# Kernel optimization log

Measured on AMD Instinct MI355X. Metric: run time of the kernel, lower is better.

Reference implementation:

```python
import jax, jax.numpy as jnp
import numpy as np

C_Z = 128
C_H = 128
N = 512
B = 1

def _layer_norm(x, g, b, eps=1e-5):
    mu = jnp.mean(x, axis=-1, keepdims=True)
    var = jnp.var(x, axis=-1, keepdims=True)
    return (x - mu) * jax.lax.rsqrt(var + eps) * g + b

def _linear(x, w, b):
    # torch Linear: y = x @ w.T + b, w: [out, in]
    return jnp.einsum('...i,oi->...o', x, w) + b

def setup_inputs() -> dict:
    key = jax.random.key(0)
    ks = jax.random.split(key, 8)
    s = 1.0 / np.sqrt(C_Z)
    return {
        'z': jax.random.normal(ks[0], (B, N, N, C_Z), jnp.float32),
        'mask': jnp.ones((B, N, N), jnp.float32),
        'ln_in_g': jnp.ones((C_Z,), jnp.float32),
        'ln_in_b': jnp.zeros((C_Z,), jnp.float32),
        'w_ag': jax.random.normal(ks[1], (C_H, C_Z), jnp.float32) * s,
        'b_ag': jnp.ones((C_H,), jnp.float32),
        'w_ap': jax.random.normal(ks[2], (C_H, C_Z), jnp.float32) * s,
        'b_ap': jnp.zeros((C_H,), jnp.float32),
        'w_bg': jax.random.normal(ks[3], (C_H, C_Z), jnp.float32) * s,
        'b_bg': jnp.ones((C_H,), jnp.float32),
        'w_bp': jax.random.normal(ks[4], (C_H, C_Z), jnp.float32) * s,
        'b_bp': jnp.zeros((C_H,), jnp.float32),
        'w_g': jax.random.normal(ks[5], (C_Z, C_Z), jnp.float32) * s,
        'b_g': jnp.zeros((C_Z,), jnp.float32),
        'w_z': jax.random.normal(ks[6], (C_Z, C_H), jnp.float32) * s,
        'b_z': jnp.zeros((C_Z,), jnp.float32),
        'ln_out_g': jnp.ones((C_H,), jnp.float32),
        'ln_out_b': jnp.zeros((C_H,), jnp.float32),
    }

def reference(z, mask, ln_in_g, ln_in_b, w_ag, b_ag, w_ap, b_ap,
              w_bg, b_bg, w_bp, b_bp, w_g, b_g, w_z, b_z,
              ln_out_g, ln_out_b):
    m = mask[..., None]                       # [B,N,N,1]
    zn = _layer_norm(z, ln_in_g, ln_in_b)     # [B,N,N,Cz]
    a = m * jax.nn.sigmoid(_linear(zn, w_ag, b_ag)) * _linear(zn, w_ap, b_ap)
    b = m * jax.nn.sigmoid(_linear(zn, w_bg, b_bg)) * _linear(zn, w_bp, b_bp)
    # outgoing: x[b,i,j,c] = sum_k a[b,i,k,c] * b[b,j,k,c]
    x = jnp.einsum('bikc,bjkc->bijc', a, b)
    x = _layer_norm(x, ln_out_g, ln_out_b)
    x = _linear(x, w_z, b_z)
    g = jax.nn.sigmoid(_linear(zn, w_g, b_g))
    return x * g
```

## Files before the change

kernel.cpp:

```cpp
#include <hip/hip_runtime.h>

#define NN 512
#define CCH 128
#define MM (NN*NN)

using f32x4  = __attribute__((ext_vector_type(4))) float;
using f32x2  = __attribute__((ext_vector_type(2))) float;
using bf16x8 = __attribute__((ext_vector_type(8))) short;
using u16x4  = __attribute__((ext_vector_type(4))) unsigned short;
typedef unsigned short u16;

__device__ __forceinline__ u16 f2bf(float f) {
    unsigned u = __builtin_bit_cast(unsigned, f);
    u += 0x7FFF + ((u >> 16) & 1);
    return (u16)(u >> 16);
}
__device__ __forceinline__ float bf2f(u16 h) {
    unsigned u = ((unsigned)h) << 16;
    return __builtin_bit_cast(float, u);
}
__device__ __forceinline__ float sigm(float x) { return 1.0f / (1.0f + __expf(-x)); }

__device__ __forceinline__ void gl_lds16(const void* g, void* l) {
    __builtin_amdgcn_global_load_lds(
        (const __attribute__((address_space(1))) void*)g,
        (__attribute__((address_space(3))) void*)l, 16, 0, 0);
}

__global__ __launch_bounds__(256) void k_prep(
    const float* __restrict__ w0, const float* __restrict__ w1,
    const float* __restrict__ w2, const float* __restrict__ w3,
    const float* __restrict__ w4, const float* __restrict__ w5,
    const float* __restrict__ b0, const float* __restrict__ b1,
    const float* __restrict__ b2, const float* __restrict__ b3,
    const float* __restrict__ b4, const float* __restrict__ b5,
    const float* __restrict__ gin, const float* __restrict__ bin,
    const float* __restrict__ gout, const float* __restrict__ bout,
    u16* __restrict__ wbf, float* __restrict__ bias2) {
    int mat = blockIdx.x;
    const float* W = mat==0?w0:mat==1?w1:mat==2?w2:mat==3?w3:mat==4?w4:w5;
    const float* B = mat==0?b0:mat==1?b1:mat==2?b2:mat==3?b3:mat==4?b4:b5;
    const float* G = (mat==5)? gout : gin;
    const float* Bt= (mat==5)? bout : bin;
    __shared__ float gs[CCH], bs[CCH];
    int tid = threadIdx.x;
    if (tid < CCH) { gs[tid] = G[tid]; bs[tid] = Bt[tid]; }
    __syncthreads();
    int o = tid >> 1, c0 = (tid & 1) * 64;
    const float* src = W + o * CCH + c0;
    char* dstrow = (char*)(wbf + mat * 16384) + o * 256;
    int key = o & 7;
    float dot = 0.f;
    #pragma unroll
    for (int q = 0; q < 16; ++q) {
        f32x4 v = *(const f32x4*)(src + q * 4);
        int c = c0 + q * 4;
        dot += bs[c]*v.x + bs[c+1]*v.y + bs[c+2]*v.z + bs[c+3]*v.w;
        u16x4 p;
        p.x = f2bf(v.x * gs[c]);     p.y = f2bf(v.y * gs[c+1]);
        p.z = f2bf(v.z * gs[c+2]);   p.w = f2bf(v.w * gs[c+3]);
        int chunk = (c0 >> 3) + (q >> 1);
        *(u16x4*)(dstrow + (((chunk ^ key)) << 4) + ((q & 1) << 3)) = p;
    }
    dot += __shfl_xor(dot, 1);
    if ((tid & 1) == 0) bias2[mat * CCH + o] = B[o] + dot;
}

__global__ __launch_bounds__(256) void k_ln(const float* __restrict__ z,
                                            u16* __restrict__ dz) {
    int tid = threadIdx.x;
    int w = tid >> 6, lane = tid & 63;
    long row = (long)blockIdx.x * 4 + w;
    f32x2 v = *(const f32x2*)(z + row * CCH + lane * 2);
    float s = v.x + v.y, s2 = v.x * v.x + v.y * v.y;
    #pragma unroll
    for (int off = 32; off; off >>= 1) {
        s  += __shfl_xor(s, off);
        s2 += __shfl_xor(s2, off);
    }
    float mu  = s * (1.0f / CCH);
    float var = s2 * (1.0f / CCH) - mu * mu;
    float rs  = rsqrtf(var + 1e-5f);
    float o0 = (v.x - mu) * rs, o1 = (v.y - mu) * rs;
    unsigned pk = (unsigned)f2bf(o0) | ((unsigned)f2bf(o1) << 16);
    *(unsigned*)(dz + row * 256 + 128 + lane * 2) = pk;
}

__global__ __launch_bounds__(256, 4) void k_proj(
    const u16* dz, const float* __restrict__ mask,
    const u16* __restrict__ wbf, const float* __restrict__ bias2,
    u16* __restrict__ aT, u16* __restrict__ bT) {
    __shared__ __align__(16) u16 w1s[8192];
    __shared__ __align__(16) u16 w2s[8192];
    int tid = threadIdx.x, w = tid >> 6, lane = tid & 63;
    int r = lane & 15, kq = lane >> 4;
    long m0 = (long)blockIdx.x * 64;
    int ch = blockIdx.y, mode = blockIdx.z;
    int i7 = (int)((m0 >> 9) & 7);
    int mat1 = (mode == 2) ? 4 : mode * 2;

    const char* W1g = (const char*)wbf + (size_t)(mat1 * 16384 + ch * 64 * CCH) * 2;
    const char* W2g = (const char*)wbf + (size_t)((mat1 + 1) * 16384 + ch * 64 * CCH) * 2;
    #pragma unroll
    for (int it = 0; it < 4; ++it) {
        long off = (long)it * 4096 + tid * 16;
        gl_lds16(W1g + off, (char*)w1s + it * 4096 + w * 1024);
        if (mode < 2) gl_lds16(W2g + off, (char*)w2s + it * 4096 + w * 1024);
    }

    bf16x8 av[4];
    long mrow = m0 + w * 16 + r;
    #pragma unroll
    for (int kb = 0; kb < 4; ++kb)
        av[kb] = *(const bf16x8*)(dz + mrow * 256 + 128 + kb * 32 + kq * 8);

    f32x4 mkv = {1.f, 1.f, 1.f, 1.f};
    if (mode < 2) mkv = *(const f32x4*)(mask + m0 + w * 16 + kq * 4);

    __syncthreads();

    f32x4 acc1[4], acc2[4];
    #pragma unroll
    for (int nt = 0; nt < 4; ++nt) { acc1[nt] = {0,0,0,0}; acc2[nt] = {0,0,0,0}; }
    #pragma unroll
    for (int nt = 0; nt < 4; ++nt) {
        int ol = nt * 16 + r;
        int key = ol & 7;
        const char* row1 = (const char*)w1s + ol * 256;
        const char* row2 = (const char*)w2s + ol * 256;
        #pragma unroll
        for (int kb = 0; kb < 4; ++kb) {
            int ph = ((kb * 4 + kq) ^ key) << 4;
            bf16x8 b1 = *(const bf16x8*)(row1 + ph);
            acc1[nt] = __builtin_amdgcn_mfma_f32_16x16x32_bf16(av[kb], b1, acc1[nt], 0, 0, 0);
            if (mode < 2) {
                bf16x8 b2 = *(const bf16x8*)(row2 + ph);
                acc2[nt] = __builtin_amdgcn_mfma_f32_16x16x32_bf16(av[kb], b2, acc2[nt], 0, 0, 0);
            }
        }
    }
    __syncthreads();
    u16* tb = w1s;

    if (mode < 2) {
        int ml0 = w * 16 + kq * 4;
        #pragma unroll
        for (int nt = 0; nt < 4; ++nt) {
            int ccl = nt * 16 + r;
            float b1v = bias2[mat1 * CCH + ch * 64 + ccl];
            float b2v = bias2[(mat1 + 1) * CCH + ch * 64 + ccl];
            u16x4 p;
            #pragma unroll
            for (int j = 0; j < 4; ++j)
                p[j] = f2bf(mkv[j] * sigm(acc1[nt][j] + b1v) * (acc2[nt][j] + b2v));
            *(u16x4*)((char*)tb + ccl * 128 + ((ml0 * 2) ^ ((ccl & 7) << 4))) = p;
        }
        __syncthreads();
        u16* dst = mode ? bT : aT;
        int ccl = tid >> 2, q2 = (tid & 3) * 2;
        const char* srow = (const char*)tb + ccl * 128;
        int key = ccl & 7;
        char* gdst = (char*)(dst + ((long)(ch * 64 + ccl)) * MM) + m0 * 2;
        #pragma unroll
        for (int e = 0; e < 2; ++e) {
            int q = q2 + e;
            bf16x8 v = *(const bf16x8*)(srow + ((q ^ key) << 4));
            *(bf16x8*)(gdst + ((q ^ i7) << 4)) = v;
        }
    } else {
        #pragma unroll
        for (int nt = 0; nt < 4; ++nt) {
            int ccl = nt * 16 + r;
            float b1v = bias2[4 * CCH + ch * 64 + ccl];
            #pragma unroll
            for (int j = 0; j < 4; ++j) {
                int ml = w * 16 + kq * 4 + j;
                *(u16*)((char*)tb + ml * 128 + ((ccl * 2) ^ ((ml & 7) << 4))) =
                    f2bf(sigm(acc1[nt][j] + b1v));
            }
        }
        __syncthreads();
        int ml = tid >> 2, q2 = (tid & 3) * 2;
        const char* srow = (const char*)tb + ml * 128;
        int key = ml & 7;
        char* grow = (char*)(dz + (m0 + ml) * 256 + ch * 64);
        #pragma unroll
        for (int e = 0; e < 2; ++e) {
            int q = q2 + e;
            bf16x8 v = *(const bf16x8*)(srow + ((q ^ key) << 4));
            *(bf16x8*)(grow + q * 16) = v;
        }
    }
}

__global__ __launch_bounds__(256, 4) void k_tri(const u16* __restrict__ aT,
                                                const u16* __restrict__ bT,
                                                u16* __restrict__ xT) {
    __shared__ __align__(16) u16 At[128 * 64];
    __shared__ __align__(16) u16 Bt[128 * 64];
    int tid = threadIdx.x;
    int w = tid >> 6, lane = tid & 63;
    int r = lane & 15, kq = lane >> 4;

    int L = blockIdx.x;
    int xcd = L & 7, idx = L >> 3;
    int c    = xcd + 8 * (idx >> 4);
    int tile = idx & 15;
    int ti = tile >> 2, tj = tile & 3;

    const char* abase = (const char*)(aT + (long)c * MM) + (long)(ti * 128) * 1024;
    const char* bbase = (const char*)(bT + (long)c * MM) + (long)(tj * 128) * 1024;
    int wm = w >> 1, wn = w & 1;

    f32x4 acc[4][4];
    #pragma unroll
    for (int a = 0; a < 4; ++a)
        #pragma unroll
        for (int bq = 0; bq < 4; ++bq) acc[a][bq] = {0.f,0.f,0.f,0.f};

    for (int ks = 0; ks < 8; ++ks) {
        const char* asrc = abase + ks * 128;
        const char* bsrc = bbase + ks * 128;
        #pragma unroll
        for (int it = 0; it < 4; ++it) {
            int u = it * 256 + tid;
            long goff = (long)(u >> 3) * 1024 + (u & 7) * 16;
            gl_lds16(asrc + goff, (char*)At + it * 4096 + w * 1024);
            gl_lds16(bsrc + goff, (char*)Bt + it * 4096 + w * 1024);
        }
        __syncthreads();

        #pragma unroll
        for (int kh = 0; kh < 2; ++kh) {
            bf16x8 af[4];
            #pragma unroll
            for (int mt = 0; mt < 4; ++mt) {
                int rowa = wm * 64 + mt * 16 + r;
                af[mt] = *(const bf16x8*)((const char*)At + rowa * 128 +
                                          (((kh * 4 + kq) ^ (r & 7)) << 4));
            }
            #pragma unroll
            for (int nt = 0; nt < 4; ++nt) {
                int rowb = wn * 64 + nt * 16 + r;
                bf16x8 bf = *(const bf16x8*)((const char*)Bt + rowb * 128 +
                                             (((kh * 4 + kq) ^ (r & 7)) << 4));
                #pragma unroll
                for (int mt = 0; mt < 4; ++mt)
                    acc[mt][nt] = __builtin_amdgcn_mfma_f32_16x16x32_bf16(af[mt], bf, acc[mt][nt], 0, 0, 0);
            }
        }
        __syncthreads();
    }

    u16* xbase = xT + (long)c * MM;
    int gi0 = ti * 128 + wm * 64;
    int gj0 = tj * 128 + wn * 64 + r;
    #pragma unroll
    for (int mt = 0; mt < 4; ++mt)
        #pragma unroll
        for (int nt = 0; nt < 4; ++nt)
            #pragma unroll
            for (int j = 0; j < 4; ++j) {
                long gi = gi0 + mt * 16 + kq * 4 + j;
                xbase[gi * NN + gj0 + nt * 16] = f2bf(acc[mt][nt][j]);
            }
}

__global__ __launch_bounds__(256, 4) void k_out(const u16* __restrict__ xT,
                                                const u16* __restrict__ wbf,
                                                const float* __restrict__ bias2,
                                                const u16* gateB,
                                                float* outp) {
    __shared__ __align__(16) u16 xl[64 * 128];
    int tid = threadIdx.x, w = tid >> 6, lane = tid & 63;
    int r = lane & 15, kq = lane >> 4;
    long m0 = (long)blockIdx.x * 64;

    {
        int cg = tid & 31, ms = tid >> 5;
        int c0 = cg * 4;
        const u16* base = xT + m0 + (long)ms * 8;
        bf16x8 v0 = *(const bf16x8*)(base + (long)(c0 + 0) * MM);
        bf16x8 v1 = *(const bf16x8*)(base + (long)(c0 + 1) * MM);
        bf16x8 v2 = *(const bf16x8*)(base + (long)(c0 + 2) * MM);
        bf16x8 v3 = *(const bf16x8*)(base + (long)(c0 + 3) * MM);
        #pragma unroll
        for (int e = 0; e < 8; ++e) {
            int m = ms * 8 + e;
            u16x4 t;
            t.x = (u16)v0[e]; t.y = (u16)v1[e]; t.z = (u16)v2[e]; t.w = (u16)v3[e];
            *(u16x4*)((char*)xl + m * 256 + ((c0 * 2) ^ ((m & 15) << 4))) = t;
        }
    }
    __syncthreads();

    int mlr = w * 16 + r;
    int swm = (mlr & 15) << 4;
    bf16x8 av[4];
    float s = 0.f, s2 = 0.f;
    #pragma unroll
    for (int kb = 0; kb < 4; ++kb) {
        av[kb] = *(const bf16x8*)((const char*)xl + mlr * 256 + ((kb * 64 + kq * 16) ^ swm));
        #pragma unroll
        for (int e = 0; e < 8; ++e) {
            float f = bf2f((u16)av[kb][e]);
            s += f; s2 += f * f;
        }
    }
    s  += __shfl_xor(s, 16);  s  += __shfl_xor(s, 32);
    s2 += __shfl_xor(s2, 16); s2 += __shfl_xor(s2, 32);
    float mu = s * (1.0f / CCH);
    float var = s2 * (1.0f / CCH) - mu * mu;
    float rs = rsqrtf(var + 1e-5f);
    #pragma unroll
    for (int kb = 0; kb < 4; ++kb)
        #pragma unroll
        for (int e = 0; e < 8; ++e) {
            float f = (bf2f((u16)av[kb][e]) - mu) * rs;
            av[kb][e] = (short)f2bf(f);
        }

    u16 gv[8][4];
    #pragma unroll
    for (int nt = 0; nt < 8; ++nt)
        #pragma unroll
        for (int j = 0; j < 4; ++j) {
            long m = m0 + w * 16 + kq * 4 + j;
            gv[nt][j] = gateB[m * 256 + nt * 16 + r];
        }

    const char* Wz = (const char*)(wbf + 5 * 16384);
    f32x4 acc[8];
    #pragma unroll
    for (int nt = 0; nt < 8; ++nt) acc[nt] = {0,0,0,0};
    #pragma unroll
    for (int nt = 0; nt < 8; ++nt) {
        int ol = nt * 16 + r;
        int key = ol & 7;
        const char* row = Wz + ol * 256;
        #pragma unroll
        for (int kb = 0; kb < 4; ++kb) {
            bf16x8 bw = *(const bf16x8*)(row + (((kb * 4 + kq) ^ key) << 4));
            acc[nt] = __builtin_amdgcn_mfma_f32_16x16x32_bf16(av[kb], bw, acc[nt], 0, 0, 0);
        }
    }

    __syncthreads();

    const float* b2z = bias2 + 5 * CCH;
    #pragma unroll
    for (int nt = 0; nt < 8; ++nt) {
        int cc = nt * 16 + r;
        float bb = b2z[cc];
        #pragma unroll
        for (int j = 0; j < 4; ++j) {
            long m = m0 + w * 16 + kq * 4 + j;
            outp[m * CCH + cc] = (acc[nt][j] + bb) * bf2f(gv[nt][j]);
        }
    }
}

extern "C" void kernel_launch(void* const* d_in, const int* in_sizes, int n_in,
                              void* d_out, int out_size, void* d_ws, size_t ws_size,
                              hipStream_t stream) {
    const float* z       = (const float*)d_in[0];
    const float* mask    = (const float*)d_in[1];
    const float* ln_in_g = (const float*)d_in[2];
    const float* ln_in_b = (const float*)d_in[3];
    const float* w_ag    = (const float*)d_in[4];
    const float* b_ag    = (const float*)d_in[5];
    const float* w_ap    = (const float*)d_in[6];
    const float* b_ap    = (const float*)d_in[7];
    const float* w_bg    = (const float*)d_in[8];
    const float* b_bg    = (const float*)d_in[9];
    const float* w_bp    = (const float*)d_in[10];
    const float* b_bp    = (const float*)d_in[11];
    const float* w_g     = (const float*)d_in[12];
    const float* b_g     = (const float*)d_in[13];
    const float* w_z     = (const float*)d_in[14];
    const float* b_z     = (const float*)d_in[15];
    const float* ln_o_g  = (const float*)d_in[16];
    const float* ln_o_b  = (const float*)d_in[17];
    float* out = (float*)d_out;
    u16* dz = (u16*)d_out;

    char* ws = (char*)d_ws;
    const size_t SL = (size_t)MM * CCH * 2;
    u16* xT   = (u16*)ws;
    u16* aT   = (u16*)(ws + SL);
    u16* bT   = (u16*)(ws + 2 * SL);
    u16* wbf  = (u16*)(ws + 3 * SL);
    float* b2 = (float*)(ws + 3 * SL + 6 * 16384 * 2);

    k_prep<<<6, 256, 0, stream>>>(w_ag, w_ap, w_bg, w_bp, w_g, w_z,
                                  b_ag, b_ap, b_bg, b_bp, b_g, b_z,
                                  ln_in_g, ln_in_b, ln_o_g, ln_o_b, wbf, b2);
    k_ln<<<MM / 4, 256, 0, stream>>>(z, dz);
    k_proj<<<dim3(MM / 64, 2, 3), 256, 0, stream>>>(dz, mask, wbf, b2, aT, bT);
    k_tri<<<2048, 256, 0, stream>>>(aT, bT, xT);
    k_out<<<MM / 64, 256, 0, stream>>>(xT, wbf, b2, dz, out);
}
```

Before: 335.1 us.

## Swap MFMA operands to emit contiguous vector stores and drop LDS transposes

```diff
diff --git a/kernel.cpp b/kernel.cpp
--- a/kernel.cpp
+++ b/kernel.cpp
@@ -8,6 +8,8 @@
 using f32x2  = __attribute__((ext_vector_type(2))) float;
 using bf16x8 = __attribute__((ext_vector_type(8))) short;
 using u16x4  = __attribute__((ext_vector_type(4))) unsigned short;
+using u32x2  = __attribute__((ext_vector_type(2))) unsigned int;
+using u32x4  = __attribute__((ext_vector_type(4))) unsigned int;
 typedef unsigned short u16;
 
 __device__ __forceinline__ u16 f2bf(float f) {
@@ -18,6 +20,9 @@
 __device__ __forceinline__ float bf2f(u16 h) {
     unsigned u = ((unsigned)h) << 16;
     return __builtin_bit_cast(float, u);
+}
+__device__ __forceinline__ unsigned pack2(float lo, float hi) {
+    return (unsigned)f2bf(lo) | ((unsigned)f2bf(hi) << 16);
 }
 __device__ __forceinline__ float sigm(float x) { return 1.0f / (1.0f + __expf(-x)); }
 
@@ -79,10 +84,9 @@
         s2 += __shfl_xor(s2, off);
     }
     float mu  = s * (1.0f / CCH);
-    float var = s2 * (1.0f / CCH) - mu * mu;
+    float var = fmaxf(s2 * (1.0f / CCH) - mu * mu, 0.f);
     float rs  = rsqrtf(var + 1e-5f);
-    float o0 = (v.x - mu) * rs, o1 = (v.y - mu) * rs;
-    unsigned pk = (unsigned)f2bf(o0) | ((unsigned)f2bf(o1) << 16);
+    unsigned pk = pack2((v.x - mu) * rs, (v.y - mu) * rs);
     *(unsigned*)(dz + row * 256 + 128 + lane * 2) = pk;
 }
 
@@ -119,76 +123,64 @@
 
     __syncthreads();
 
-    f32x4 acc1[4], acc2[4];
-    #pragma unroll
-    for (int nt = 0; nt < 4; ++nt) { acc1[nt] = {0,0,0,0}; acc2[nt] = {0,0,0,0}; }
-    #pragma unroll
-    for (int nt = 0; nt < 4; ++nt) {
-        int ol = nt * 16 + r;
-        int key = ol & 7;
-        const char* row1 = (const char*)w1s + ol * 256;
-        const char* row2 = (const char*)w2s + ol * 256;
-        #pragma unroll
-        for (int kb = 0; kb < 4; ++kb) {
-            int ph = ((kb * 4 + kq) ^ key) << 4;
-            bf16x8 b1 = *(const bf16x8*)(row1 + ph);
-            acc1[nt] = __builtin_amdgcn_mfma_f32_16x16x32_bf16(av[kb], b1, acc1[nt], 0, 0, 0);
-            if (mode < 2) {
+    if (mode < 2) {
+        f32x4 acc1[4], acc2[4];
+        #pragma unroll
+        for (int nt = 0; nt < 4; ++nt) { acc1[nt] = {0,0,0,0}; acc2[nt] = {0,0,0,0}; }
+        #pragma unroll
+        for (int nt = 0; nt < 4; ++nt) {
+            int ol = nt * 16 + r;
+            int key = ol & 7;
+            const char* row1 = (const char*)w1s + ol * 256;
+            const char* row2 = (const char*)w2s + ol * 256;
+            #pragma unroll
+            for (int kb = 0; kb < 4; ++kb) {
+                int ph = ((kb * 4 + kq) ^ key) << 4;
+                bf16x8 b1 = *(const bf16x8*)(row1 + ph);
                 bf16x8 b2 = *(const bf16x8*)(row2 + ph);
+                acc1[nt] = __builtin_amdgcn_mfma_f32_16x16x32_bf16(av[kb], b1, acc1[nt], 0, 0, 0);
                 acc2[nt] = __builtin_amdgcn_mfma_f32_16x16x32_bf16(av[kb], b2, acc2[nt], 0, 0, 0);
             }
         }
-    }
-    __syncthreads();
-    u16* tb = w1s;
-
-    if (mode < 2) {
-        int ml0 = w * 16 + kq * 4;
+        u16* dst = mode ? bT : aT;
+        int q = w * 2 + (kq >> 1);
+        long boff = m0 * 2 + (long)((q ^ i7) << 4) + ((kq & 1) << 3);
         #pragma unroll
         for (int nt = 0; nt < 4; ++nt) {
-            int ccl = nt * 16 + r;
-            float b1v = bias2[mat1 * CCH + ch * 64 + ccl];
-            float b2v = bias2[(mat1 + 1) * CCH + ch * 64 + ccl];
-            u16x4 p;
+            int cc = nt * 16 + r;
+            float b1v = bias2[mat1 * CCH + ch * 64 + cc];
+            float b2v = bias2[(mat1 + 1) * CCH + ch * 64 + cc];
+            float v0 = mkv[0] * sigm(acc1[nt][0] + b1v) * (acc2[nt][0] + b2v);
+            float v1 = mkv[1] * sigm(acc1[nt][1] + b1v) * (acc2[nt][1] + b2v);
+            float v2 = mkv[2] * sigm(acc1[nt][2] + b1v) * (acc2[nt][2] + b2v);
+            float v3 = mkv[3] * sigm(acc1[nt][3] + b1v) * (acc2[nt][3] + b2v);
+            u32x2 pv; pv.x = pack2(v0, v1); pv.y = pack2(v2, v3);
+            *(u32x2*)((char*)(dst + (long)(ch * 64 + cc) * MM) + boff) = pv;
+        }
+    } else {
+        f32x4 acc[4];
+        #pragma unroll
+        for (int nt = 0; nt < 4; ++nt) acc[nt] = {0,0,0,0};
+        #pragma unroll
+        for (int nt = 0; nt < 4; ++nt) {
+            int ol = nt * 16 + r;
+            int key = ol & 7;
+            const char* row1 = (const char*)w1s + ol * 256;
             #pragma unroll
-            for (int j = 0; j < 4; ++j)
-                p[j] = f2bf(mkv[j] * sigm(acc1[nt][j] + b1v) * (acc2[nt][j] + b2v));
-            *(u16x4*)((char*)tb + ccl * 128 + ((ml0 * 2) ^ ((ccl & 7) << 4))) = p;
-        }
-        __syncthreads();
-        u16* dst = mode ? bT : aT;
-        int ccl = tid >> 2, q2 = (tid & 3) * 2;
-        const char* srow = (const char*)tb + ccl * 128;
-        int key = ccl & 7;
-        char* gdst = (char*)(dst + ((long)(ch * 64 + ccl)) * MM) + m0 * 2;
-        #pragma unroll
-        for (int e = 0; e < 2; ++e) {
-            int q = q2 + e;
-            bf16x8 v = *(const bf16x8*)(srow + ((q ^ key) << 4));
-            *(bf16x8*)(gdst + ((q ^ i7) << 4)) = v;
-        }
-    } else {
+            for (int kb = 0; kb < 4; ++kb) {
+                bf16x8 b1 = *(const bf16x8*)(row1 + (((kb * 4 + kq) ^ key) << 4));
+                acc[nt] = __builtin_amdgcn_mfma_f32_16x16x32_bf16(b1, av[kb], acc[nt], 0, 0, 0);
+            }
+        }
+        long m = m0 + w * 16 + r;
         #pragma unroll
         for (int nt = 0; nt < 4; ++nt) {
-            int ccl = nt * 16 + r;
-            float b1v = bias2[4 * CCH + ch * 64 + ccl];
-            #pragma unroll
-            for (int j = 0; j < 4; ++j) {
-                int ml = w * 16 + kq * 4 + j;
-                *(u16*)((char*)tb + ml * 128 + ((ccl * 2) ^ ((ml & 7) << 4))) =
-                    f2bf(sigm(acc1[nt][j] + b1v));
-            }
-        }
-        __syncthreads();
-        int ml = tid >> 2, q2 = (tid & 3) * 2;
-        const char* srow = (const char*)tb + ml * 128;
-        int key = ml & 7;
-        char* grow = (char*)(dz + (m0 + ml) * 256 + ch * 64);
-        #pragma unroll
-        for (int e = 0; e < 2; ++e) {
-            int q = q2 + e;
-            bf16x8 v = *(const bf16x8*)(srow + ((q ^ key) << 4));
-            *(bf16x8*)(grow + q * 16) = v;
+            int c0 = nt * 16 + kq * 4;
+            f32x4 bg = *(const f32x4*)(bias2 + 4 * CCH + ch * 64 + c0);
+            u32x2 pv;
+            pv.x = pack2(sigm(acc[nt][0] + bg[0]), sigm(acc[nt][1] + bg[1]));
+            pv.y = pack2(sigm(acc[nt][2] + bg[2]), sigm(acc[nt][3] + bg[3]));
+            *(u32x2*)(dz + m * 256 + ch * 64 + c0) = pv;
         }
     }
 }
@@ -246,7 +238,7 @@
                                              (((kh * 4 + kq) ^ (r & 7)) << 4));
                 #pragma unroll
                 for (int mt = 0; mt < 4; ++mt)
-                    acc[mt][nt] = __builtin_amdgcn_mfma_f32_16x16x32_bf16(af[mt], bf, acc[mt][nt], 0, 0, 0);
+                    acc[mt][nt] = __builtin_amdgcn_mfma_f32_16x16x32_bf16(bf, af[mt], acc[mt][nt], 0, 0, 0);
             }
         }
         __syncthreads();
@@ -254,23 +246,26 @@
 
     u16* xbase = xT + (long)c * MM;
     int gi0 = ti * 128 + wm * 64;
-    int gj0 = tj * 128 + wn * 64 + r;
-    #pragma unroll
-    for (int mt = 0; mt < 4; ++mt)
-        #pragma unroll
-        for (int nt = 0; nt < 4; ++nt)
-            #pragma unroll
-            for (int j = 0; j < 4; ++j) {
-                long gi = gi0 + mt * 16 + kq * 4 + j;
-                xbase[gi * NN + gj0 + nt * 16] = f2bf(acc[mt][nt][j]);
-            }
+    int gj0 = tj * 128 + wn * 64;
+    #pragma unroll
+    for (int mt = 0; mt < 4; ++mt) {
+        long row = gi0 + mt * 16 + r;
+        #pragma unroll
+        for (int nt = 0; nt < 4; ++nt) {
+            int col = gj0 + nt * 16 + kq * 4;
+            u32x2 pv;
+            pv.x = pack2(acc[mt][nt][0], acc[mt][nt][1]);
+            pv.y = pack2(acc[mt][nt][2], acc[mt][nt][3]);
+            *(u32x2*)(xbase + row * NN + col) = pv;
+        }
+    }
 }
 
 __global__ __launch_bounds__(256, 4) void k_out(const u16* __restrict__ xT,
                                                 const u16* __restrict__ wbf,
                                                 const float* __restrict__ bias2,
                                                 const u16* gateB,
-                                                float* outp) {
+                                                float* __restrict__ outp) {
     __shared__ __align__(16) u16 xl[64 * 128];
     int tid = threadIdx.x, w = tid >> 6, lane = tid & 63;
     int r = lane & 15, kq = lane >> 4;
@@ -296,38 +291,46 @@
 
     int mlr = w * 16 + r;
     int swm = (mlr & 15) << 4;
-    bf16x8 av[4];
+    u32x4 avu[4];
     float s = 0.f, s2 = 0.f;
     #pragma unroll
     for (int kb = 0; kb < 4; ++kb) {
-        av[kb] = *(const bf16x8*)((const char*)xl + mlr * 256 + ((kb * 64 + kq * 16) ^ swm));
-        #pragma unroll
-        for (int e = 0; e < 8; ++e) {
-            float f = bf2f((u16)av[kb][e]);
-            s += f; s2 += f * f;
+        avu[kb] = *(const u32x4*)((const char*)xl + mlr * 256 + ((kb * 64 + kq * 16) ^ swm));
+        #pragma unroll
+        for (int p = 0; p < 4; ++p) {
+            unsigned u = avu[kb][p];
+            float flo = __builtin_bit_cast(float, u << 16);
+            float fhi = __builtin_bit_cast(float, u & 0xFFFF0000u);
+            s += flo + fhi;
+            s2 = fmaf(flo, flo, s2);
+            s2 = fmaf(fhi, fhi, s2);
         }
     }
     s  += __shfl_xor(s, 16);  s  += __shfl_xor(s, 32);
     s2 += __shfl_xor(s2, 16); s2 += __shfl_xor(s2, 32);
     float mu = s * (1.0f / CCH);
-    float var = s2 * (1.0f / CCH) - mu * mu;
+    float var = fmaxf(s2 * (1.0f / CCH) - mu * mu, 0.f);
     float rs = rsqrtf(var + 1e-5f);
-    #pragma unroll
-    for (int kb = 0; kb < 4; ++kb)
-        #pragma unroll
-        for (int e = 0; e < 8; ++e) {
-            float f = (bf2f((u16)av[kb][e]) - mu) * rs;
-            av[kb][e] = (short)f2bf(f);
-        }
-
-    u16 gv[8][4];
+    float nmu = -mu * rs;
+    bf16x8 av[4];
+    #pragma unroll
+    for (int kb = 0; kb < 4; ++kb) {
+        u32x4 o;
+        #pragma unroll
+        for (int p = 0; p < 4; ++p) {
+            unsigned u = avu[kb][p];
+            float flo = __builtin_bit_cast(float, u << 16);
+            float fhi = __builtin_bit_cast(float, u & 0xFFFF0000u);
+            o[p] = pack2(fmaf(flo, rs, nmu), fmaf(fhi, rs, nmu));
+        }
+        av[kb] = __builtin_bit_cast(bf16x8, o);
+    }
+
+    long m = m0 + w * 16 + r;
+    u16x4 gvu[8];
     #pragma unroll
     for (int nt = 0; nt < 8; ++nt)
-        #pragma unroll
-        for (int j = 0; j < 4; ++j) {
-            long m = m0 + w * 16 + kq * 4 + j;
-            gv[nt][j] = gateB[m * 256 + nt * 16 + r];
-        }
+        gvu[nt] = *(const u16x4*)(gateB + m * 256 + nt * 16 + kq * 4);
 
     const char* Wz = (const char*)(wbf + 5 * 16384);
     f32x4 acc[8];
@@ -341,7 +344,7 @@
         #pragma unroll
         for (int kb = 0; kb < 4; ++kb) {
             bf16x8 bw = *(const bf16x8*)(row + (((kb * 4 + kq) ^ key) << 4));
-            acc[nt] = __builtin_amdgcn_mfma_f32_16x16x32_bf16(av[kb], bw, acc[nt], 0, 0, 0);
+            acc[nt] = __builtin_amdgcn_mfma_f32_16x16x32_bf16(bw, av[kb], acc[nt], 0, 0, 0);
         }
     }
 
@@ -350,13 +353,13 @@
     const float* b2z = bias2 + 5 * CCH;
     #pragma unroll
     for (int nt = 0; nt < 8; ++nt) {
-        int cc = nt * 16 + r;
-        float bb = b2z[cc];
-        #pragma unroll
-        for (int j = 0; j < 4; ++j) {
-            long m = m0 + w * 16 + kq * 4 + j;
-            outp[m * CCH + cc] = (acc[nt][j] + bb) * bf2f(gv[nt][j]);
-        }
+        int c0 = nt * 16 + kq * 4;
+        f32x4 bb = *(const f32x4*)(b2z + c0);
+        f32x4 o;
+        #pragma unroll
+        for (int j = 0; j < 4; ++j)
+            o[j] = (acc[nt][j] + bb[j]) * bf2f(gvu[nt][j]);
+        *(f32x4*)(outp + m * CCH + c0) = o;
     }
 }
 
```

Result: slower. 350.2 us (+4.5%).
